# Kernel optimization log

Measured on AMD Instinct MI355X. Metric: run time of the kernel, lower is better.

The kernel has to match this reference:

```python
import jax, jax.numpy as jnp
import numpy as np

N, E, D, L = 100000, 500000, 128, 5
NUM_ATOM_FEATS, ATOM_VOCAB = 9, 120
NUM_BOND_FEATS, BOND_VOCAB = 3, 8
BN_EPS = 1e-5


def setup_inputs() -> dict:
    key = jax.random.key(0)
    ks = jax.random.split(key, 16)
    inp = {
        "x": jax.random.randint(ks[0], (N, NUM_ATOM_FEATS), 0, ATOM_VOCAB),
        "edge_index": jax.random.randint(ks[1], (2, E), 0, N),
        "edge_attr": jax.random.randint(ks[2], (E, NUM_BOND_FEATS), 0, BOND_VOCAB),
        "edge_weight": jax.random.uniform(ks[3], (E,), dtype=jnp.float32),
        # parameters
        "atom_emb": jax.random.normal(ks[4], (NUM_ATOM_FEATS, ATOM_VOCAB, D), dtype=jnp.float32) * 0.02,
        "bond_emb": jax.random.normal(ks[5], (L, NUM_BOND_FEATS, BOND_VOCAB, D), dtype=jnp.float32) * 0.02,
        "eps": jnp.zeros((L,), dtype=jnp.float32),
        "W1": jax.random.normal(ks[6], (L, D, 2 * D), dtype=jnp.float32) / np.sqrt(D),
        "b1": jnp.zeros((L, 2 * D), dtype=jnp.float32),
        "g1": jnp.ones((L, 2 * D), dtype=jnp.float32),
        "bt1": jnp.zeros((L, 2 * D), dtype=jnp.float32),
        "W2": jax.random.normal(ks[7], (L, 2 * D, D), dtype=jnp.float32) / np.sqrt(2 * D),
        "b2": jnp.zeros((L, D), dtype=jnp.float32),
        "g_out": jnp.ones((L, D), dtype=jnp.float32),
        "bt_out": jnp.zeros((L, D), dtype=jnp.float32),
    }
    return inp


def _batchnorm(h, g, b):
    # training-mode BN over node axis, biased variance (matches torch BN normalization)
    mu = jnp.mean(h, axis=0)
    var = jnp.mean((h - mu) ** 2, axis=0)
    return g * (h - mu) * jax.lax.rsqrt(var + BN_EPS) + b


def reference(x, edge_index, edge_attr, edge_weight,
              atom_emb, bond_emb, eps, W1, b1, g1, bt1, W2, b2, g_out, bt_out):
    # AtomEncoder: sum per-column embedding lookups -> [N, D]
    h = atom_emb[jnp.arange(NUM_ATOM_FEATS)[None, :], x].sum(axis=1)
    src, dst = edge_index[0], edge_index[1]
    ew = edge_weight[:, None]
    for l in range(L):
        # BondEncoder for layer l -> [E, D]
        e = bond_emb[l][jnp.arange(NUM_BOND_FEATS)[None, :], edge_attr].sum(axis=1)
        # message: relu(x_j + edge_emb) * edge_weight ; aggregate: scatter-add at dst
        m = jax.nn.relu(h[src] + e) * ew
        agg = jax.ops.segment_sum(m, dst, num_segments=N)
        z = (1.0 + eps[l]) * h + agg
        # GIN MLP: Linear -> BN -> ReLU -> Linear
        z = jax.nn.relu(_batchnorm(z @ W1[l] + b1[l], g1[l], bt1[l])) @ W2[l] + b2[l]
        # outer BatchNorm; dropout is identity in eval mode
        h_new = _batchnorm(z, g_out[l], bt_out[l])
        h = h_new if l == L - 1 else jax.nn.relu(h_new)
    return h
```

## Files before the change

kernel.cpp:

```cpp
#include <hip/hip_runtime.h>
#include <hip/hip_bf16.h>
#include <hip/hip_fp16.h>

#define NN 100000
#define EE 500000
#define NP 100096

typedef _Float16 f16;
typedef __attribute__((ext_vector_type(8))) _Float16 f16x8;
typedef __attribute__((ext_vector_type(4))) _Float16 f16x4;
typedef __attribute__((ext_vector_type(4))) float f32x4;

static __device__ __forceinline__ f16x8 relu8(f16x8 a) {
#if __has_builtin(__builtin_elementwise_max)
  f16x8 z = {0, 0, 0, 0, 0, 0, 0, 0};
  return __builtin_elementwise_max(a, z);
#else
  f16x8 r;
#pragma unroll
  for (int i = 0; i < 8; ++i) r[i] = (a[i] > (f16)0) ? a[i] : (f16)0;
  return r;
#endif
}

__global__ __launch_bounds__(256) void prep_kernel(const float* __restrict__ W1,
                                                   const float* __restrict__ W2,
                                                   f16* __restrict__ w1f,
                                                   f16* __restrict__ w2f) {
  int gid = blockIdx.x * 256 + threadIdx.x;
  if (gid < 163840) {
    int l = gid / 32768; int rem = gid % 32768;
    int k = rem / 256;   int n = rem % 256;
    int ctg = n >> 4, m = n & 15;
    int c = k >> 5, q = (k >> 3) & 3, e = k & 7;
    int lane = q * 16 + m;
    w1f[l * 32768 + ((ctg * 4 + c) * 64 + lane) * 8 + e] = (f16)W1[gid];
  } else if (gid < 327680) {
    int g = gid - 163840;
    int l = g / 32768; int rem = g % 32768;
    int k = rem / 128; int n = rem % 128;
    int ctg = n >> 4, m = n & 15;
    int c = k >> 5, q = (k >> 3) & 3, e = k & 7;
    int lane = q * 16 + m;
    w2f[l * 32768 + ((ctg * 8 + c) * 64 + lane) * 8 + e] = (f16)W2[g];
  }
}

__global__ __launch_bounds__(256) void bondtab_kernel(const float* __restrict__ bemb,
                                                      f16* __restrict__ tab) {
  int gid = blockIdx.x * 256 + threadIdx.x;
  int l = gid >> 16;
  int rem = gid & 65535;
  int combo = rem >> 7, d = rem & 127;
  int a0 = combo & 7, a1 = (combo >> 3) & 7, a2 = combo >> 6;
  const float* bl = bemb + l * 3072;
  float v = bl[a0 * 128 + d] + bl[1024 + a1 * 128 + d] + bl[2048 + a2 * 128 + d];
  tab[gid] = (f16)v;
}

__global__ __launch_bounds__(256) void zero_deg_kernel(int* __restrict__ deg) {
  int i = blockIdx.x * 256 + threadIdx.x;
  if (i < NN) deg[i] = 0;
}

__global__ __launch_bounds__(256) void hist_kernel(const int* __restrict__ ei, int* __restrict__ deg) {
  int e = blockIdx.x * 256 + threadIdx.x;
  if (e < EE) atomicAdd(&deg[ei[EE + e]], 1);
}

__global__ __launch_bounds__(256) void scan1_kernel(const int* __restrict__ deg,
                                                    int* __restrict__ offs,
                                                    int* __restrict__ bsum) {
  __shared__ int sh[256];
  int b = blockIdx.x, t = threadIdx.x;
  int base = b * 1024 + t * 4;
  int v[4];
  int s = 0;
#pragma unroll
  for (int i = 0; i < 4; ++i) { v[i] = (base + i < NN) ? deg[base + i] : 0; s += v[i]; }
  sh[t] = s;
  __syncthreads();
  for (int off = 1; off < 256; off <<= 1) {
    int x = (t >= off) ? sh[t - off] : 0;
    __syncthreads();
    sh[t] += x;
    __syncthreads();
  }
  int excl = sh[t] - s;
  if (t == 255) bsum[b] = sh[255];
  int run = excl;
#pragma unroll
  for (int i = 0; i < 4; ++i) {
    if (base + i < NN) offs[base + i] = run;
    run += v[i];
  }
}

__global__ void scan2_kernel(int* __restrict__ bsum, int nb) {
  if (threadIdx.x == 0 && blockIdx.x == 0) {
    int run = 0;
    for (int i = 0; i < nb; ++i) { int v = bsum[i]; bsum[i] = run; run += v; }
  }
}

__global__ __launch_bounds__(256) void scan3_kernel(int* __restrict__ offs,
                                                    const int* __restrict__ bsum,
                                                    int* __restrict__ cursor) {
  int i = blockIdx.x * 256 + threadIdx.x;
  if (i < NN) {
    int v = offs[i] + bsum[i >> 10];
    offs[i] = v;
    cursor[i] = v;
  } else if (i == NN) {
    offs[NN] = EE;
  }
}

__global__ __launch_bounds__(256) void scatter_kernel(const int* __restrict__ ei,
                                                      const int* __restrict__ ea,
                                                      const float* __restrict__ ew,
                                                      int* __restrict__ cursor,
                                                      int* __restrict__ pk,
                                                      float* __restrict__ wsrt) {
  int e = blockIdx.x * 256 + threadIdx.x;
  if (e >= EE) return;
  int dst = ei[EE + e];
  int pos = atomicAdd(&cursor[dst], 1);
  int src = ei[e];
  int a0 = ea[e * 3 + 0], a1 = ea[e * 3 + 1], a2 = ea[e * 3 + 2];
  pk[pos] = src | (a0 << 17) | (a1 << 20) | (a2 << 23);
  wsrt[pos] = ew[e];
}

__global__ __launch_bounds__(256) void zero_slices_kernel(float* __restrict__ p) {
  int i = blockIdx.x * 256 + threadIdx.x;
  *(float4*)(p + i * 4) = float4{0.f, 0.f, 0.f, 0.f};
}

__global__ __launch_bounds__(256) void atom_kernel(const int* __restrict__ x,
                                                   const float* __restrict__ aemb,
                                                   f16* __restrict__ hf) {
  int gid = blockIdx.x * 256 + threadIdx.x;
  int n = gid >> 5, qq = gid & 31;
  if (n >= NN) return;
  float4 s = {0.f, 0.f, 0.f, 0.f};
#pragma unroll
  for (int f = 0; f < 9; ++f) {
    int xi = x[n * 9 + f];
    float4 v = *(const float4*)(aemb + (f * 120 + xi) * 128 + qq * 4);
    s.x += v.x; s.y += v.y; s.z += v.z; s.w += v.w;
  }
  f16x4 o;
  o[0] = (f16)s.x; o[1] = (f16)s.y; o[2] = (f16)s.z; o[3] = (f16)s.w;
  *(f16x4*)(hf + (long)n * 128 + qq * 4) = o;
}

__global__ __launch_bounds__(256) void edge_agg_kernel(const int* __restrict__ offs,
                                                       const int* __restrict__ pk,
                                                       const float* __restrict__ wsrt,
                                                       const f16* __restrict__ tab,
                                                       const float* __restrict__ eps,
                                                       const f16* __restrict__ hf,
                                                       f16* __restrict__ zb) {
  int gid = blockIdx.x * 256 + threadIdx.x;
  int n = gid >> 4, d0 = (gid & 15) * 8;
  if (n >= NN) {
    f16x8 z = {0, 0, 0, 0, 0, 0, 0, 0};
    *(f16x8*)(zb + (long)n * 128 + d0) = z;
    return;
  }
  int s0 = offs[n], s1 = offs[n + 1];
  float e1 = 1.f + eps[0];
  f16x8 hn = *(const f16x8*)(hf + (long)n * 128 + d0);
  float acc[8];
#pragma unroll
  for (int i = 0; i < 8; ++i) acc[i] = e1 * (float)hn[i];

  int e = s0;
  int pc; float wc; f16x8 hc, bc;
  if (e < s1) {
    pc = pk[e]; wc = wsrt[e];
    hc = *(const f16x8*)(hf + (long)(pc & 131071) * 128 + d0);
    bc = *(const f16x8*)(tab + ((pc >> 17) & 511) * 128 + d0);
  }
  for (; e < s1; ++e) {
    int en = e + 1;
    bool more = en < s1;
    int pn; float wn; f16x8 hx, bx;
    if (more) {
      pn = pk[en]; wn = wsrt[en];
      hx = *(const f16x8*)(hf + (long)(pn & 131071) * 128 + d0);
      bx = *(const f16x8*)(tab + ((pn >> 17) & 511) * 128 + d0);
    }
    f16x8 sm = relu8(hc + bc);
#pragma unroll
    for (int i = 0; i < 8; ++i) acc[i] += (float)sm[i] * wc;
    if (more) { pc = pn; wc = wn; hc = hx; bc = bx; }
  }
  f16x8 o;
#pragma unroll
  for (int i = 0; i < 8; ++i) o[i] = (f16)acc[i];
  *(f16x8*)(zb + (long)n * 128 + d0) = o;
}

__global__ __launch_bounds__(256) void edge_agg_bn_kernel(const int* __restrict__ offs,
                                                          const int* __restrict__ pk,
                                                          const float* __restrict__ wsrt,
                                                          const f16* __restrict__ tab,
                                                          const float* __restrict__ eps, int l,
                                                          const f16* __restrict__ t2,
                                                          const float* __restrict__ sum2s,
                                                          const float* __restrict__ sq2s,
                                                          const float* __restrict__ g2,
                                                          const float* __restrict__ bt2,
                                                          float* __restrict__ s1z,
                                                          f16* __restrict__ zb) {
  __shared__ float sc2[128], sh2[128];
  const int tid = threadIdx.x;
  if (tid < 128) {
    float s = 0.f, s2 = 0.f;
#pragma unroll
    for (int k = 0; k < 16; ++k) { s += sum2s[k * 128 + tid]; s2 += sq2s[k * 128 + tid]; }
    float mu = s * (1.f / NN);
    float var = fmaxf(s2 * (1.f / NN) - mu * mu, 0.f);
    float is = rsqrtf(var + 1e-5f);
    float sc = g2[tid] * is;
    sc2[tid] = sc;
    sh2[tid] = bt2[tid] - mu * sc;
  }
  if (blockIdx.x == 0) {
#pragma unroll
    for (int j = 0; j < 8; ++j)
      *(float4*)(s1z + (j * 256 + tid) * 4) = float4{0.f, 0.f, 0.f, 0.f};
  }
  __syncthreads();
  int gid = blockIdx.x * 256 + tid;
  int n = gid >> 4, d0 = (gid & 15) * 8;
  if (n >= NN) {
    f16x8 z = {0, 0, 0, 0, 0, 0, 0, 0};
    *(f16x8*)(zb + (long)n * 128 + d0) = z;
    return;
  }
  float4 svA = *(const float4*)(sc2 + d0), svB = *(const float4*)(sc2 + d0 + 4);
  float4 shA = *(const float4*)(sh2 + d0), shB = *(const float4*)(sh2 + d0 + 4);
  float sv[8] = {svA.x, svA.y, svA.z, svA.w, svB.x, svB.y, svB.z, svB.w};
  float hv[8] = {shA.x, shA.y, shA.z, shA.w, shB.x, shB.y, shB.z, shB.w};
  f16x8 sv8, hv8;
#pragma unroll
  for (int i = 0; i < 8; ++i) { sv8[i] = (f16)sv[i]; hv8[i] = (f16)hv[i]; }

  int s0 = offs[n], s1 = offs[n + 1];
  float e1 = 1.f + eps[l];
  f16x8 hn = *(const f16x8*)(t2 + (long)n * 128 + d0);
  float acc[8];
#pragma unroll
  for (int i = 0; i < 8; ++i)
    acc[i] = e1 * fmaxf((float)hn[i] * sv[i] + hv[i], 0.f);

  int e = s0;
  int pc; float wc; f16x8 hc, bc;
  if (e < s1) {
    pc = pk[e]; wc = wsrt[e];
    hc = *(const f16x8*)(t2 + (long)(pc & 131071) * 128 + d0);
    bc = *(const f16x8*)(tab + ((pc >> 17) & 511) * 128 + d0);
  }
  for (; e < s1; ++e) {
    int en = e + 1;
    bool more = en < s1;
    int pn; float wn; f16x8 hx, bx;
    if (more) {
      pn = pk[en]; wn = wsrt[en];
      hx = *(const f16x8*)(t2 + (long)(pn & 131071) * 128 + d0);
      bx = *(const f16x8*)(tab + ((pn >> 17) & 511) * 128 + d0);
    }
    f16x8 y = relu8(hc * sv8 + hv8);
    f16x8 sm = relu8(y + bc);
#pragma unroll
    for (int i = 0; i < 8; ++i) acc[i] += (float)sm[i] * wc;
    if (more) { pc = pn; wc = wn; hc = hx; bc = bx; }
  }
  f16x8 o;
#pragma unroll
  for (int i = 0; i < 8; ++i) o[i] = (f16)acc[i];
  *(f16x8*)(zb + (long)n * 128 + d0) = o;
}

__global__ __launch_bounds__(256) void gemm1_kernel(const f16* __restrict__ zb,
                                                    const f16* __restrict__ w1f,
                                                    f16* __restrict__ t1f,
                                                    float* __restrict__ sum1s,
                                                    float* __restrict__ sq1s,
                                                    float* __restrict__ s2z) {
  __shared__ __align__(16) char ldsraw[17408];
  const int tid = threadIdx.x;
  const int lane = tid & 63, w = tid >> 6;
  const int wr = w >> 1, wc = w & 1;
  const int m = lane & 15, q = lane >> 4;
  const int cb = blockIdx.x;
  const int rbase = blockIdx.y * 64;
  const int slice = blockIdx.y & 15;

  if (blockIdx.y == 0 && cb == 0) {
#pragma unroll
    for (int j = 0; j < 4; ++j)
      *(float4*)(s2z + (j * 256 + tid) * 4) = float4{0.f, 0.f, 0.f, 0.f};
  }

  f16x8 B[4][4];
#pragma unroll
  for (int ct = 0; ct < 4; ++ct)
#pragma unroll
    for (int c = 0; c < 4; ++c)
      B[ct][c] = *(const f16x8*)(w1f + (((cb * 8 + wc * 4 + ct) * 4 + c) * 64 + lane) * 8);

  {
    f16x8 st[4];
    const int tofs = tid * 16;
#pragma unroll
    for (int j = 0; j < 4; ++j)
      st[j] = *(const f16x8*)(zb + (long)rbase * 128 + (tofs + j * 4096) / 2);
#pragma unroll
    for (int j = 0; j < 4; ++j) {
      int ofs = tofs + j * 4096;
      int row = ofs >> 8, colb = ofs & 255;
      *(f16x8*)(ldsraw + row * 256 + (colb ^ ((row & 7) << 4))) = st[j];
    }
  }
  __syncthreads();

  f16x8 A[2][4];
#pragma unroll
  for (int rt = 0; rt < 2; ++rt) {
    int row = wr * 32 + rt * 16 + m;
    int rs = row * 256, sw = (row & 7) << 4;
#pragma unroll
    for (int c = 0; c < 4; ++c) {
      int colb = c * 64 + q * 16;
      A[rt][c] = *(const f16x8*)(ldsraw + rs + (colb ^ sw));
    }
  }

  f32x4 acc[2][4];
  const f32x4 zf = {0.f, 0.f, 0.f, 0.f};
#pragma unroll
  for (int a = 0; a < 2; ++a)
#pragma unroll
    for (int b = 0; b < 4; ++b) acc[a][b] = zf;

#pragma unroll
  for (int c = 0; c < 4; ++c)
#pragma unroll
    for (int rt = 0; rt < 2; ++rt)
#pragma unroll
      for (int ct = 0; ct < 4; ++ct)
        acc[rt][ct] = __builtin_amdgcn_mfma_f32_16x16x32_f16(A[rt][c], B[ct][c], acc[rt][ct], 0, 0, 0);

  __syncthreads();
  f16 (*sh)[136] = (f16(*)[136])ldsraw;

#pragma unroll
  for (int ct = 0; ct < 4; ++ct) {
    int lc = wc * 64 + ct * 16 + m;
    int gc = cb * 128 + lc;
    float s = 0.f, s2 = 0.f;
#pragma unroll
    for (int rt = 0; rt < 2; ++rt) {
      int lr = wr * 32 + rt * 16 + q * 4;
#pragma unroll
      for (int i = 0; i < 4; ++i) {
        float v = acc[rt][ct][i];
        s += v; s2 += v * v;
        sh[lr + i][lc] = (f16)v;
      }
    }
    s  += __shfl_xor(s, 16);  s  += __shfl_xor(s, 32);
    s2 += __shfl_xor(s2, 16); s2 += __shfl_xor(s2, 32);
    if (q == 0) {
      unsafeAtomicAdd(&sum1s[slice * 256 + gc], s);
      unsafeAtomicAdd(&sq1s[slice * 256 + gc], s2);
    }
  }
  __syncthreads();
  const int colc = tid & 15, r0 = tid >> 4;
#pragma unroll
  for (int j = 0; j < 4; ++j) {
    int r = j * 16 + r0;
    f16x8 v = *(const f16x8*)(&sh[r][colc * 8]);
    *(f16x8*)(t1f + (long)(rbase + r) * 256 + cb * 128 + colc * 8) = v;
  }
}

__global__ __launch_bounds__(256) void gemm2_kernel(const f16* __restrict__ a1,
                                                    const f16* __restrict__ w2f,
                                                    const float* __restrict__ sum1s,
                                                    const float* __restrict__ sq1s,
                                                    const float* __restrict__ g1,
                                                    const float* __restrict__ bt1,
                                                    f16* __restrict__ t2out,
                                                    float* __restrict__ sum2s,
                                                    float* __restrict__ sq2s) {
  __shared__ __align__(16) char ldsraw[34816];
  float* sc1 = (float*)(ldsraw + 32768);
  float* sh1 = (float*)(ldsraw + 33792);
  const int tid = threadIdx.x;
  const int lane = tid & 63, w = tid >> 6;
  const int wr = w >> 1, wc = w & 1;
  const int m = lane & 15, q = lane >> 4;
  const int rbase = blockIdx.x * 64;
  const int slice = blockIdx.x & 15;

  f16x8 st[8];
  const int tofs = tid * 16;
#pragma unroll
  for (int j = 0; j < 8; ++j)
    st[j] = *(const f16x8*)(a1 + (long)rbase * 256 + (tofs + j * 4096) / 2);

  {
    float s = 0.f, s2 = 0.f;
#pragma unroll
    for (int k = 0; k < 16; ++k) { s += sum1s[k * 256 + tid]; s2 += sq1s[k * 256 + tid]; }
    float mu = s * (1.f / NN);
    float var = fmaxf(s2 * (1.f / NN) - mu * mu, 0.f);
    float is = rsqrtf(var + 1e-5f);
    float sc = g1[tid] * is;
    sc1[tid] = sc;
    sh1[tid] = bt1[tid] - mu * sc;
  }
  __syncthreads();

  {
    const int k0 = (tid & 31) * 8;
    float4 sa = *(const float4*)(sc1 + k0);
    float4 sb = *(const float4*)(sc1 + k0 + 4);
    float4 ha = *(const float4*)(sh1 + k0);
    float4 hb = *(const float4*)(sh1 + k0 + 4);
#pragma unroll
    for (int j = 0; j < 8; ++j) {
      int ofs = tofs + j * 4096;
      int row = ofs >> 9, colb = ofs & 511;
      f16x8 u = st[j], o;
      o[0] = (f16)fmaxf((float)u[0] * sa.x + ha.x, 0.f);
      o[1] = (f16)fmaxf((float)u[1] * sa.y + ha.y, 0.f);
      o[2] = (f16)fmaxf((float)u[2] * sa.z + ha.z, 0.f);
      o[3] = (f16)fmaxf((float)u[3] * sa.w + ha.w, 0.f);
      o[4] = (f16)fmaxf((float)u[4] * sb.x + hb.x, 0.f);
      o[5] = (f16)fmaxf((float)u[5] * sb.y + hb.y, 0.f);
      o[6] = (f16)fmaxf((float)u[6] * sb.z + hb.z, 0.f);
      o[7] = (f16)fmaxf((float)u[7] * sb.w + hb.w, 0.f);
      *(f16x8*)(ldsraw + row * 512 + (colb ^ ((row & 7) << 4))) = o;
    }
  }
  __syncthreads();

  f32x4 acc[2][4];
  const f32x4 zf = {0.f, 0.f, 0.f, 0.f};
#pragma unroll
  for (int a = 0; a < 2; ++a)
#pragma unroll
    for (int b = 0; b < 4; ++b) acc[a][b] = zf;

#pragma unroll
  for (int hh = 0; hh < 2; ++hh) {
    f16x8 A[2][4], B[4][4];
#pragma unroll
    for (int rt = 0; rt < 2; ++rt) {
      int row = wr * 32 + rt * 16 + m;
      int rs = row * 512, sw = (row & 7) << 4;
#pragma unroll
      for (int c = 0; c < 4; ++c) {
        int colb = (hh * 4 + c) * 64 + q * 16;
        A[rt][c] = *(const f16x8*)(ldsraw + rs + (colb ^ sw));
      }
    }
#pragma unroll
    for (int ct = 0; ct < 4; ++ct)
#pragma unroll
      for (int c = 0; c < 4; ++c)
        B[ct][c] = *(const f16x8*)(w2f + (((wc * 4 + ct) * 8 + hh * 4 + c) * 64 + lane) * 8);
#pragma unroll
    for (int c = 0; c < 4; ++c)
#pragma unroll
      for (int rt = 0; rt < 2; ++rt)
#pragma unroll
        for (int ct = 0; ct < 4; ++ct)
          acc[rt][ct] = __builtin_amdgcn_mfma_f32_16x16x32_f16(A[rt][c], B[ct][c], acc[rt][ct], 0, 0, 0);
  }

  __syncthreads();
  f16 (*sh)[136] = (f16(*)[136])ldsraw;

#pragma unroll
  for (int ct = 0; ct < 4; ++ct) {
    int gc = wc * 64 + ct * 16 + m;
    float s = 0.f, s2 = 0.f;
#pragma unroll
    for (int rt = 0; rt < 2; ++rt) {
      int grow = rbase + wr * 32 + rt * 16 + q * 4;
      int lr = wr * 32 + rt * 16 + q * 4;
#pragma unroll
      for (int i = 0; i < 4; ++i) {
        float v = acc[rt][ct][i];
        float vv = (grow + i < NN) ? v : 0.f;
        s += vv; s2 += vv * vv;
        sh[lr + i][gc] = (f16)v;
      }
    }
    s  += __shfl_xor(s, 16);  s  += __shfl_xor(s, 32);
    s2 += __shfl_xor(s2, 16); s2 += __shfl_xor(s2, 32);
    if (q == 0) {
      unsafeAtomicAdd(&sum2s[slice * 128 + gc], s);
      unsafeAtomicAdd(&sq2s[slice * 128 + gc], s2);
    }
  }
  __syncthreads();
  const int colc = tid & 15, r0 = tid >> 4;
#pragma unroll
  for (int j = 0; j < 4; ++j) {
    int r = j * 16 + r0;
    f16x8 v = *(const f16x8*)(&sh[r][colc * 8]);
    *(f16x8*)(t2out + (long)(rbase + r) * 128 + colc * 8) = v;
  }
}

__global__ __launch_bounds__(256) void apply_kernel(const f16* __restrict__ t2,
                                                    const float* __restrict__ sum2s,
                                                    const float* __restrict__ sq2s,
                                                    const float* __restrict__ g2,
                                                    const float* __restrict__ bt2,
                                                    float* __restrict__ outp) {
  __shared__ float sc2[128], sh2[128];
  const int tid = threadIdx.x;
  if (tid < 128) {
    float s = 0.f, s2 = 0.f;
#pragma unroll
    for (int k = 0; k < 16; ++k) { s += sum2s[k * 128 + tid]; s2 += sq2s[k * 128 + tid]; }
    float mu = s * (1.f / NN);
    float var = fmaxf(s2 * (1.f / NN) - mu * mu, 0.f);
    float is = rsqrtf(var + 1e-5f);
    float sc = g2[tid] * is;
    sc2[tid] = sc;
    sh2[tid] = bt2[tid] - mu * sc;
  }
  __syncthreads();
  const int rbase = blockIdx.x * 64;
#pragma unroll
  for (int k = 0; k < 4; ++k) {
    int ci = tid + k * 256;
    int r = ci >> 4, c8 = ci & 15;
    int row = rbase + r;
    if (row >= NN) continue;
    f16x8 u = *(const f16x8*)(t2 + (long)row * 128 + c8 * 8);
    float4 sa = *(const float4*)(sc2 + c8 * 8);
    float4 sb = *(const float4*)(sc2 + c8 * 8 + 4);
    float4 ha = *(const float4*)(sh2 + c8 * 8);
    float4 hb = *(const float4*)(sh2 + c8 * 8 + 4);
    float4 o0 = {(float)u[0] * sa.x + ha.x, (float)u[1] * sa.y + ha.y,
                 (float)u[2] * sa.z + ha.z, (float)u[3] * sa.w + ha.w};
    float4 o1 = {(float)u[4] * sb.x + hb.x, (float)u[5] * sb.y + hb.y,
                 (float)u[6] * sb.z + hb.z, (float)u[7] * sb.w + hb.w};
    *(float4*)(outp + (long)row * 128 + c8 * 8) = o0;
    *(float4*)(outp + (long)row * 128 + c8 * 8 + 4) = o1;
  }
}

extern "C" void kernel_launch(void* const* d_in, const int* in_sizes, int n_in,
                              void* d_out, int out_size, void* d_ws, size_t ws_size,
                              hipStream_t stream) {
  (void)in_sizes; (void)n_in; (void)out_size; (void)ws_size;
  const int*   x      = (const int*)d_in[0];
  const int*   ei     = (const int*)d_in[1];
  const int*   ea     = (const int*)d_in[2];
  const float* ew     = (const float*)d_in[3];
  const float* aemb   = (const float*)d_in[4];
  const float* bemb   = (const float*)d_in[5];
  const float* eps    = (const float*)d_in[6];
  const float* W1     = (const float*)d_in[7];
  const float* g1     = (const float*)d_in[9];
  const float* bt1    = (const float*)d_in[10];
  const float* W2     = (const float*)d_in[11];
  const float* g_out  = (const float*)d_in[13];
  const float* bt_out = (const float*)d_in[14];

  float* outp = (float*)d_out;

  char* ws = (char*)d_ws;
  f16*   hf    = (f16*)(ws);
  f16*   zb    = (f16*)(ws + 25624576);
  f16*   t1f   = (f16*)(ws + 51249152);
  f16*   w1f   = (f16*)(ws + 102498304);
  f16*   w2f   = (f16*)(ws + 102825984);
  float* slices= (float*)(ws + 103153664);
  int*   offs  = (int*)(ws + 103202816);
  int*   bsum  = (int*)(ws + 103602848);
  int*   deg   = (int*)(ws + 103603360);
  int*   cursor= (int*)(ws + 104003360);
  f16*   bsumtab = (f16*)(ws + 103603360);
  int*   pk    = (int*)(ws + 104403360);
  float* wsrt  = (float*)(ws + 106403360);

  float* sum1s = slices;
  float* sq1s  = slices + 4096;
  float* sum2s = slices + 8192;
  float* sq2s  = slices + 10240;

  prep_kernel<<<1280, 256, 0, stream>>>(W1, W2, w1f, w2f);
  zero_deg_kernel<<<391, 256, 0, stream>>>(deg);
  hist_kernel<<<1954, 256, 0, stream>>>(ei, deg);
  scan1_kernel<<<98, 256, 0, stream>>>(deg, offs, bsum);
  scan2_kernel<<<1, 64, 0, stream>>>(bsum, 98);
  scan3_kernel<<<392, 256, 0, stream>>>(offs, bsum, cursor);
  scatter_kernel<<<1954, 256, 0, stream>>>(ei, ea, ew, cursor, pk, wsrt);
  bondtab_kernel<<<1280, 256, 0, stream>>>(bemb, bsumtab);
  zero_slices_kernel<<<12, 256, 0, stream>>>(slices);
  atom_kernel<<<12500, 256, 0, stream>>>(x, aemb, hf);

  for (int l = 0; l < 5; ++l) {
    if (l == 0) {
      edge_agg_kernel<<<6256, 256, 0, stream>>>(offs, pk, wsrt, bsumtab, eps, hf, zb);
    } else {
      edge_agg_bn_kernel<<<6256, 256, 0, stream>>>(offs, pk, wsrt, bsumtab + l * 65536, eps, l,
                                                   hf, sum2s, sq2s,
                                                   g_out + (l - 1) * 128, bt_out + (l - 1) * 128,
                                                   sum1s, zb);
    }
    gemm1_kernel<<<dim3(2, 1564), 256, 0, stream>>>(zb, w1f + l * 32768, t1f, sum1s, sq1s, sum2s);
    gemm2_kernel<<<1564, 256, 0, stream>>>(t1f, w2f + l * 32768, sum1s, sq1s,
                                           g1 + l * 256, bt1 + l * 256, hf, sum2s, sq2s);
    if (l == 4)
      apply_kernel<<<1564, 256, 0, stream>>>(hf, sum2s, sq2s, g_out + 512, bt_out + 512, outp);
  }
}
```

Measured before the change: 598.4 us.

## Recompute first GEMM instead of storing intermediate; fuse BN1+ReLU+GEMM2

Replaces the gemm1/gemm2 pair with a stats-only first pass that computes Z@W1 just for the batch-norm statistics, and a fused MLP kernel that recomputes Z@W1, applies BN1 and ReLU in registers, writes the result to LDS, and runs the second GEMM. This removes the write and read-back of the N×256 fp16 intermediate through global memory. In exchange the first GEMM is computed twice, and the fused kernel uses more LDS (50 KB) with reduced occupancy.

```diff
diff --git a/kernel.cpp b/kernel.cpp
--- a/kernel.cpp
+++ b/kernel.cpp
@@ -285,123 +285,12 @@
   *(f16x8*)(zb + (long)n * 128 + d0) = o;
 }
 
-__global__ __launch_bounds__(256) void gemm1_kernel(const f16* __restrict__ zb,
-                                                    const f16* __restrict__ w1f,
-                                                    f16* __restrict__ t1f,
-                                                    float* __restrict__ sum1s,
-                                                    float* __restrict__ sq1s,
-                                                    float* __restrict__ s2z) {
-  __shared__ __align__(16) char ldsraw[17408];
-  const int tid = threadIdx.x;
-  const int lane = tid & 63, w = tid >> 6;
-  const int wr = w >> 1, wc = w & 1;
-  const int m = lane & 15, q = lane >> 4;
-  const int cb = blockIdx.x;
-  const int rbase = blockIdx.y * 64;
-  const int slice = blockIdx.y & 15;
-
-  if (blockIdx.y == 0 && cb == 0) {
-#pragma unroll
-    for (int j = 0; j < 4; ++j)
-      *(float4*)(s2z + (j * 256 + tid) * 4) = float4{0.f, 0.f, 0.f, 0.f};
-  }
-
-  f16x8 B[4][4];
-#pragma unroll
-  for (int ct = 0; ct < 4; ++ct)
-#pragma unroll
-    for (int c = 0; c < 4; ++c)
-      B[ct][c] = *(const f16x8*)(w1f + (((cb * 8 + wc * 4 + ct) * 4 + c) * 64 + lane) * 8);
-
-  {
-    f16x8 st[4];
-    const int tofs = tid * 16;
-#pragma unroll
-    for (int j = 0; j < 4; ++j)
-      st[j] = *(const f16x8*)(zb + (long)rbase * 128 + (tofs + j * 4096) / 2);
-#pragma unroll
-    for (int j = 0; j < 4; ++j) {
-      int ofs = tofs + j * 4096;
-      int row = ofs >> 8, colb = ofs & 255;
-      *(f16x8*)(ldsraw + row * 256 + (colb ^ ((row & 7) << 4))) = st[j];
-    }
-  }
-  __syncthreads();
-
-  f16x8 A[2][4];
-#pragma unroll
-  for (int rt = 0; rt < 2; ++rt) {
-    int row = wr * 32 + rt * 16 + m;
-    int rs = row * 256, sw = (row & 7) << 4;
-#pragma unroll
-    for (int c = 0; c < 4; ++c) {
-      int colb = c * 64 + q * 16;
-      A[rt][c] = *(const f16x8*)(ldsraw + rs + (colb ^ sw));
-    }
-  }
-
-  f32x4 acc[2][4];
-  const f32x4 zf = {0.f, 0.f, 0.f, 0.f};
-#pragma unroll
-  for (int a = 0; a < 2; ++a)
-#pragma unroll
-    for (int b = 0; b < 4; ++b) acc[a][b] = zf;
-
-#pragma unroll
-  for (int c = 0; c < 4; ++c)
-#pragma unroll
-    for (int rt = 0; rt < 2; ++rt)
-#pragma unroll
-      for (int ct = 0; ct < 4; ++ct)
-        acc[rt][ct] = __builtin_amdgcn_mfma_f32_16x16x32_f16(A[rt][c], B[ct][c], acc[rt][ct], 0, 0, 0);
-
-  __syncthreads();
-  f16 (*sh)[136] = (f16(*)[136])ldsraw;
-
-#pragma unroll
-  for (int ct = 0; ct < 4; ++ct) {
-    int lc = wc * 64 + ct * 16 + m;
-    int gc = cb * 128 + lc;
-    float s = 0.f, s2 = 0.f;
-#pragma unroll
-    for (int rt = 0; rt < 2; ++rt) {
-      int lr = wr * 32 + rt * 16 + q * 4;
-#pragma unroll
-      for (int i = 0; i < 4; ++i) {
-        float v = acc[rt][ct][i];
-        s += v; s2 += v * v;
-        sh[lr + i][lc] = (f16)v;
-      }
-    }
-    s  += __shfl_xor(s, 16);  s  += __shfl_xor(s, 32);
-    s2 += __shfl_xor(s2, 16); s2 += __shfl_xor(s2, 32);
-    if (q == 0) {
-      unsafeAtomicAdd(&sum1s[slice * 256 + gc], s);
-      unsafeAtomicAdd(&sq1s[slice * 256 + gc], s2);
-    }
-  }
-  __syncthreads();
-  const int colc = tid & 15, r0 = tid >> 4;
-#pragma unroll
-  for (int j = 0; j < 4; ++j) {
-    int r = j * 16 + r0;
-    f16x8 v = *(const f16x8*)(&sh[r][colc * 8]);
-    *(f16x8*)(t1f + (long)(rbase + r) * 256 + cb * 128 + colc * 8) = v;
-  }
-}
-
-__global__ __launch_bounds__(256) void gemm2_kernel(const f16* __restrict__ a1,
-                                                    const f16* __restrict__ w2f,
-                                                    const float* __restrict__ sum1s,
-                                                    const float* __restrict__ sq1s,
-                                                    const float* __restrict__ g1,
-                                                    const float* __restrict__ bt1,
-                                                    f16* __restrict__ t2out,
-                                                    float* __restrict__ sum2s,
-                                                    float* __restrict__ sq2s) {
-  __shared__ __align__(16) char ldsraw[34816];
-  float* sc1 = (float*)(ldsraw + 32768);
-  float* sh1 = (float*)(ldsraw + 33792);
+__global__ __launch_bounds__(256) void stats1_kernel(const f16* __restrict__ zb,
+                                                     const f16* __restrict__ w1f,
+                                                     float* __restrict__ sum1s,
+                                                     float* __restrict__ sq1s,
+                                                     float* __restrict__ s2z) {
+  __shared__ __align__(16) char ldsraw[16384];
   const int tid = threadIdx.x;
   const int lane = tid & 63, w = tid >> 6;
   const int wr = w >> 1, wc = w & 1;
@@ -409,11 +298,110 @@
   const int rbase = blockIdx.x * 64;
   const int slice = blockIdx.x & 15;
 
-  f16x8 st[8];
+  if (blockIdx.x == 0) {
+#pragma unroll
+    for (int j = 0; j < 4; ++j)
+      *(float4*)(s2z + (j * 256 + tid) * 4) = float4{0.f, 0.f, 0.f, 0.f};
+  }
+
+  {
+    f16x8 st[4];
+    const int tofs = tid * 16;
+#pragma unroll
+    for (int j = 0; j < 4; ++j)
+      st[j] = *(const f16x8*)(zb + (long)rbase * 128 + (tofs + j * 4096) / 2);
+#pragma unroll
+    for (int j = 0; j < 4; ++j) {
+      int ofs = tofs + j * 4096;
+      int row = ofs >> 8, colb = ofs & 255;
+      *(f16x8*)(ldsraw + row * 256 + (colb ^ ((row & 7) << 4))) = st[j];
+    }
+  }
+  __syncthreads();
+
+  f16x8 A[2][4];
+#pragma unroll
+  for (int rt = 0; rt < 2; ++rt) {
+    int row = wr * 32 + rt * 16 + m;
+    int rs = row * 256, sw = (row & 7) << 4;
+#pragma unroll
+    for (int c = 0; c < 4; ++c) {
+      int colb = c * 64 + q * 16;
+      A[rt][c] = *(const f16x8*)(ldsraw + rs + (colb ^ sw));
+    }
+  }
+
+#pragma unroll
+  for (int h = 0; h < 2; ++h) {
+    f16x8 B[4][4];
+#pragma unroll
+    for (int ct = 0; ct < 4; ++ct)
+#pragma unroll
+      for (int c = 0; c < 4; ++c)
+        B[ct][c] = *(const f16x8*)(w1f + (((h * 8 + wc * 4 + ct) * 4 + c) * 64 + lane) * 8);
+
+    f32x4 acc[2][4];
+    const f32x4 zf = {0.f, 0.f, 0.f, 0.f};
+#pragma unroll
+    for (int a = 0; a < 2; ++a)
+#pragma unroll
+      for (int b = 0; b < 4; ++b) acc[a][b] = zf;
+#pragma unroll
+    for (int c = 0; c < 4; ++c)
+#pragma unroll
+      for (int rt = 0; rt < 2; ++rt)
+#pragma unroll
+        for (int ct = 0; ct < 4; ++ct)
+          acc[rt][ct] = __builtin_amdgcn_mfma_f32_16x16x32_f16(A[rt][c], B[ct][c], acc[rt][ct], 0, 0, 0);
+
+#pragma unroll
+    for (int ct = 0; ct < 4; ++ct) {
+      int gc = h * 128 + wc * 64 + ct * 16 + m;
+      float s = 0.f, s2 = 0.f;
+#pragma unroll
+      for (int rt = 0; rt < 2; ++rt)
+#pragma unroll
+        for (int i = 0; i < 4; ++i) {
+          float v = acc[rt][ct][i];
+          s += v; s2 += v * v;
+        }
+      s  += __shfl_xor(s, 16);  s  += __shfl_xor(s, 32);
+      s2 += __shfl_xor(s2, 16); s2 += __shfl_xor(s2, 32);
+      if (q == 0) {
+        unsafeAtomicAdd(&sum1s[slice * 256 + gc], s);
+        unsafeAtomicAdd(&sq1s[slice * 256 + gc], s2);
+      }
+    }
+  }
+}
+
+__global__ __launch_bounds__(256, 3) void mlp_kernel(const f16* __restrict__ zb,
+                                                     const f16* __restrict__ w1f,
+                                                     const f16* __restrict__ w2f,
+                                                     const float* __restrict__ sum1s,
+                                                     const float* __restrict__ sq1s,
+                                                     const float* __restrict__ g1,
+                                                     const float* __restrict__ bt1,
+                                                     f16* __restrict__ t2out,
+                                                     float* __restrict__ sum2s,
+                                                     float* __restrict__ sq2s) {
+  __shared__ __align__(16) char lds[51200];
+  float* sc1 = (float*)(lds + 49152 - 1024 + 1024);
+  float* sh1 = (float*)(lds + 49152 + 1024 - 1024 + 1024);
+  sc1 = (float*)(lds + 48 * 1024);
+  sh1 = (float*)(lds + 49 * 1024);
+  const int tid = threadIdx.x;
+  const int lane = tid & 63, w = tid >> 6;
+  const int wr = w >> 1, wc = w & 1;
+  const int m = lane & 15, q = lane >> 4;
+  const int rbase = blockIdx.x * 64;
+  const int slice = blockIdx.x & 15;
+
+  f16x8 st[4];
   const int tofs = tid * 16;
 #pragma unroll
-  for (int j = 0; j < 8; ++j)
-    st[j] = *(const f16x8*)(a1 + (long)rbase * 256 + (tofs + j * 4096) / 2);
+  for (int j = 0; j < 4; ++j)
+    st[j] = *(const f16x8*)(zb + (long)rbase * 128 + (tofs + j * 4096) / 2);
 
   {
     float s = 0.f, s2 = 0.f;
@@ -426,68 +414,105 @@
     sc1[tid] = sc;
     sh1[tid] = bt1[tid] - mu * sc;
   }
-  __syncthreads();
-
-  {
-    const int k0 = (tid & 31) * 8;
-    float4 sa = *(const float4*)(sc1 + k0);
-    float4 sb = *(const float4*)(sc1 + k0 + 4);
-    float4 ha = *(const float4*)(sh1 + k0);
-    float4 hb = *(const float4*)(sh1 + k0 + 4);
-#pragma unroll
-    for (int j = 0; j < 8; ++j) {
-      int ofs = tofs + j * 4096;
-      int row = ofs >> 9, colb = ofs & 511;
-      f16x8 u = st[j], o;
-      o[0] = (f16)fmaxf((float)u[0] * sa.x + ha.x, 0.f);
-      o[1] = (f16)fmaxf((float)u[1] * sa.y + ha.y, 0.f);
-      o[2] = (f16)fmaxf((float)u[2] * sa.z + ha.z, 0.f);
-      o[3] = (f16)fmaxf((float)u[3] * sa.w + ha.w, 0.f);
-      o[4] = (f16)fmaxf((float)u[4] * sb.x + hb.x, 0.f);
-      o[5] = (f16)fmaxf((float)u[5] * sb.y + hb.y, 0.f);
-      o[6] = (f16)fmaxf((float)u[6] * sb.z + hb.z, 0.f);
-      o[7] = (f16)fmaxf((float)u[7] * sb.w + hb.w, 0.f);
-      *(f16x8*)(ldsraw + row * 512 + (colb ^ ((row & 7) << 4))) = o;
-    }
-  }
-  __syncthreads();
-
-  f32x4 acc[2][4];
-  const f32x4 zf = {0.f, 0.f, 0.f, 0.f};
+
+#pragma unroll
+  for (int j = 0; j < 4; ++j) {
+    int ofs = tofs + j * 4096;
+    int row = ofs >> 8, colb = ofs & 255;
+    *(f16x8*)(lds + row * 256 + (colb ^ ((row & 7) << 4))) = st[j];
+  }
+  __syncthreads();
+
+  f16x8 A1[2][4];
+#pragma unroll
+  for (int rt = 0; rt < 2; ++rt) {
+    int row = wr * 32 + rt * 16 + m;
+    int rs = row * 256, sw = (row & 7) << 4;
+#pragma unroll
+    for (int c = 0; c < 4; ++c) {
+      int colb = c * 64 + q * 16;
+      A1[rt][c] = *(const f16x8*)(lds + rs + (colb ^ sw));
+    }
+  }
+
+#pragma unroll
+  for (int h = 0; h < 2; ++h) {
+    f16x8 B[4][4];
+#pragma unroll
+    for (int ct = 0; ct < 4; ++ct)
+#pragma unroll
+      for (int c = 0; c < 4; ++c)
+        B[ct][c] = *(const f16x8*)(w1f + (((h * 8 + wc * 4 + ct) * 4 + c) * 64 + lane) * 8);
+
+    f32x4 acc[2][4];
+    const f32x4 zf = {0.f, 0.f, 0.f, 0.f};
+#pragma unroll
+    for (int a = 0; a < 2; ++a)
+#pragma unroll
+      for (int b = 0; b < 4; ++b) acc[a][b] = zf;
+#pragma unroll
+    for (int c = 0; c < 4; ++c)
+#pragma unroll
+      for (int rt = 0; rt < 2; ++rt)
+#pragma unroll
+        for (int ct = 0; ct < 4; ++ct)
+          acc[rt][ct] = __builtin_amdgcn_mfma_f32_16x16x32_f16(A1[rt][c], B[ct][c], acc[rt][ct], 0, 0, 0);
+
+#pragma unroll
+    for (int ct = 0; ct < 4; ++ct) {
+      int gcol = h * 128 + wc * 64 + ct * 16 + m;
+      float sc = sc1[gcol], shv = sh1[gcol];
+      int cb2 = 2 * gcol;
+#pragma unroll
+      for (int rt = 0; rt < 2; ++rt) {
+        int lr0 = wr * 32 + rt * 16 + q * 4;
+#pragma unroll
+        for (int i = 0; i < 4; ++i) {
+          int row = lr0 + i;
+          f16 o = (f16)fmaxf(acc[rt][ct][i] * sc + shv, 0.f);
+          *(f16*)(lds + 16384 + row * 512 + (cb2 ^ ((row & 7) << 4))) = o;
+        }
+      }
+    }
+  }
+  __syncthreads();
+
+  f32x4 acc2[2][4];
+  const f32x4 zf2 = {0.f, 0.f, 0.f, 0.f};
 #pragma unroll
   for (int a = 0; a < 2; ++a)
 #pragma unroll
-    for (int b = 0; b < 4; ++b) acc[a][b] = zf;
+    for (int b = 0; b < 4; ++b) acc2[a][b] = zf2;
 
 #pragma unroll
   for (int hh = 0; hh < 2; ++hh) {
-    f16x8 A[2][4], B[4][4];
+    f16x8 A2[2][4], B2[4][4];
 #pragma unroll
     for (int rt = 0; rt < 2; ++rt) {
       int row = wr * 32 + rt * 16 + m;
-      int rs = row * 512, sw = (row & 7) << 4;
+      int rs = 16384 + row * 512, sw = (row & 7) << 4;
 #pragma unroll
       for (int c = 0; c < 4; ++c) {
         int colb = (hh * 4 + c) * 64 + q * 16;
-        A[rt][c] = *(const f16x8*)(ldsraw + rs + (colb ^ sw));
+        A2[rt][c] = *(const f16x8*)(lds + rs + (colb ^ sw));
       }
     }
 #pragma unroll
     for (int ct = 0; ct < 4; ++ct)
 #pragma unroll
       for (int c = 0; c < 4; ++c)
-        B[ct][c] = *(const f16x8*)(w2f + (((wc * 4 + ct) * 8 + hh * 4 + c) * 64 + lane) * 8);
+        B2[ct][c] = *(const f16x8*)(w2f + (((wc * 4 + ct) * 8 + hh * 4 + c) * 64 + lane) * 8);
 #pragma unroll
     for (int c = 0; c < 4; ++c)
 #pragma unroll
       for (int rt = 0; rt < 2; ++rt)
 #pragma unroll
         for (int ct = 0; ct < 4; ++ct)
-          acc[rt][ct] = __builtin_amdgcn_mfma_f32_16x16x32_f16(A[rt][c], B[ct][c], acc[rt][ct], 0, 0, 0);
-  }
-
-  __syncthreads();
-  f16 (*sh)[136] = (f16(*)[136])ldsraw;
+          acc2[rt][ct] = __builtin_amdgcn_mfma_f32_16x16x32_f16(A2[rt][c], B2[ct][c], acc2[rt][ct], 0, 0, 0);
+  }
+
+  __syncthreads();
+  f16 (*sh)[136] = (f16(*)[136])lds;
 
 #pragma unroll
   for (int ct = 0; ct < 4; ++ct) {
@@ -499,7 +524,7 @@
       int lr = wr * 32 + rt * 16 + q * 4;
 #pragma unroll
       for (int i = 0; i < 4; ++i) {
-        float v = acc[rt][ct][i];
+        float v = acc2[rt][ct][i];
         float vv = (grow + i < NN) ? v : 0.f;
         s += vv; s2 += vv * vv;
         sh[lr + i][gc] = (f16)v;
@@ -586,7 +611,6 @@
   char* ws = (char*)d_ws;
   f16*   hf    = (f16*)(ws);
   f16*   zb    = (f16*)(ws + 25624576);
-  f16*   t1f   = (f16*)(ws + 51249152);
   f16*   w1f   = (f16*)(ws + 102498304);
   f16*   w2f   = (f16*)(ws + 102825984);
   float* slices= (float*)(ws + 103153664);
@@ -623,9 +647,10 @@
                                                    g_out + (l - 1) * 128, bt_out + (l - 1) * 128,
                                                    sum1s, zb);
     }
-    gemm1_kernel<<<dim3(2, 1564), 256, 0, stream>>>(zb, w1f + l * 32768, t1f, sum1s, sq1s, sum2s);
-    gemm2_kernel<<<1564, 256, 0, stream>>>(t1f, w2f + l * 32768, sum1s, sq1s,
-                                           g1 + l * 256, bt1 + l * 256, hf, sum2s, sq2s);
+    stats1_kernel<<<1564, 256, 0, stream>>>(zb, w1f + l * 32768, sum1s, sq1s, sum2s);
+    mlp_kernel<<<1564, 256, 0, stream>>>(zb, w1f + l * 32768, w2f + l * 32768,
+                                         sum1s, sq1s, g1 + l * 256, bt1 + l * 256,
+                                         hf, sum2s, sq2s);
     if (l == 4)
       apply_kernel<<<1564, 256, 0, stream>>>(hf, sum2s, sq2s, g_out + 512, bt_out + 512, outp);
   }
```

Result: slower. 616.9 us (+3.1%).
